# Performance work log

Measured on AMD Instinct MI355X. Metric: run time of the kernel, lower is better.

Reference implementation:

```python
import jax, jax.numpy as jnp
import numpy as np

N, E = 20000, 160000
F, H, OUT = 256, 8, 128
L = 6            # total layers -> 5 GAT layers
LM1 = L - 1
NGN = L // 3 + 1 # 3 GraphNorms
D = F // H       # 32 per head
GN_FREQ = 3
EPS = 1e-5


def setup_inputs() -> dict:
    key = jax.random.key(0)
    ks = jax.random.split(key, 12)
    x = jax.random.normal(ks[0], (N, 1), dtype=jnp.float32)
    edge_index = jax.random.randint(ks[1], (2, E), 0, N, dtype=jnp.int32)
    W0 = jax.random.normal(ks[2], (1, F), dtype=jnp.float32) * 0.1
    b0 = jnp.zeros((F,), jnp.float32)
    gat_lin = jax.random.normal(ks[3], (LM1, F, F), dtype=jnp.float32) * (1.0 / np.sqrt(F))
    att_src = jax.random.normal(ks[4], (LM1, H, D), dtype=jnp.float32) * 0.1
    att_dst = jax.random.normal(ks[5], (LM1, H, D), dtype=jnp.float32) * 0.1
    gat_bias = jnp.zeros((LM1, F), jnp.float32)
    gn_weight = jnp.ones((NGN, F), jnp.float32)
    gn_bias = jnp.zeros((NGN, F), jnp.float32)
    gn_mean_scale = jnp.ones((NGN, F), jnp.float32)
    lin_W = jax.random.normal(ks[6], (F, OUT), dtype=jnp.float32) * (1.0 / np.sqrt(F))
    lin_b = jnp.zeros((OUT,), jnp.float32)
    return {"x": x, "W0": W0, "b0": b0, "gat_lin": gat_lin, "att_src": att_src,
            "att_dst": att_dst, "gat_bias": gat_bias, "gn_weight": gn_weight,
            "gn_bias": gn_bias, "gn_mean_scale": gn_mean_scale,
            "lin_W": lin_W, "lin_b": lin_b, "edge_index": edge_index}


def _gcn_conv(x, W, b, src, dst, n):
    h = x @ W
    deg = jax.ops.segment_sum(jnp.ones(src.shape[0], h.dtype), dst, num_segments=n)
    dinv = jnp.where(deg > 0, jax.lax.rsqrt(deg), 0.0)
    norm = dinv[src] * dinv[dst]                      # [E']
    out = jax.ops.segment_sum(h[src] * norm[:, None], dst, num_segments=n)
    return out + b


def _gat_conv(x, W, a_src, a_dst, src, dst, n):
    # PyG GATConv (concat=True, negative_slope=0.2, self-loops in src/dst)
    h = (x @ W).reshape(n, H, D)
    s = jnp.einsum('nhd,hd->nh', h, a_src)            # [N,H]
    t = jnp.einsum('nhd,hd->nh', h, a_dst)
    e = jax.nn.leaky_relu(s[src] + t[dst], 0.2)       # [E',H]
    m = jax.ops.segment_max(e, dst, num_segments=n)   # per-dst softmax
    e = jnp.exp(e - m[dst])
    denom = jax.ops.segment_sum(e, dst, num_segments=n)
    alpha = e / (denom[dst] + 1e-16)
    out = jax.ops.segment_sum(h[src] * alpha[:, :, None], dst, num_segments=n)
    return out.reshape(n, F)


def _graph_norm(x, w, b, ms):
    # PyG GraphNorm with batch=None (single graph): per-feature stats over nodes
    mean = jnp.mean(x, axis=0)
    out = x - ms * mean
    var = jnp.mean(out * out, axis=0)
    return w * out * jax.lax.rsqrt(var + EPS) + b


def reference(x, W0, b0, gat_lin, att_src, att_dst, gat_bias, gn_weight, gn_bias,
              gn_mean_scale, lin_W, lin_b, edge_index):
    n = x.shape[0]
    loops = jnp.arange(n, dtype=edge_index.dtype)
    src = jnp.concatenate([edge_index[0], loops])
    dst = jnp.concatenate([edge_index[1], loops])
    h = jax.nn.relu(_gcn_conv(x, W0, b0, src, dst, n))
    for i in range(LM1):
        if i % GN_FREQ == 0:
            g = i // GN_FREQ
            h = _graph_norm(h, gn_weight[g], gn_bias[g], gn_mean_scale[g])
        out = _gat_conv(h, gat_lin[i], att_src[i], att_dst[i], src, dst, n)
        if i % GN_FREQ == 0:
            out = out + gat_bias[i]
        h = h + jax.nn.relu(out)
    return h @ lin_W + lin_b
```

## Files before the change

kernel.cpp:

```cpp
#include <hip/hip_runtime.h>
#include <hip/hip_bf16.h>
#include <stdint.h>

typedef float f32x4 __attribute__((ext_vector_type(4)));
typedef short s16x8 __attribute__((ext_vector_type(8)));

__device__ __forceinline__ float bf2f(unsigned short u) {
    union { unsigned int i; float f; } v; v.i = ((unsigned int)u) << 16; return v.f;
}
__device__ __forceinline__ unsigned short f2bf(float f) {
    union { float f; unsigned int i; } v; v.f = f;
    unsigned int x = v.i;
    return (unsigned short)((x + 0x7fffu + ((x >> 16) & 1u)) >> 16);
}
__device__ __forceinline__ void bfp(unsigned int u, float& lo, float& hi) {
    union { unsigned int i; float f; } a, b;
    a.i = u << 16; b.i = u & 0xffff0000u;
    lo = a.f; hi = b.f;
}
__device__ __forceinline__ void gload16(const void* g, void* l) {
    __builtin_amdgcn_global_load_lds(
        (const __attribute__((address_space(1))) void*)g,
        (__attribute__((address_space(3))) void*)l, 16, 0, 0);
}

__global__ void k_count(const int* __restrict__ ei, int E, int* deg) {
    int e = blockIdx.x * blockDim.x + threadIdx.x;
    if (e < E) atomicAdd(&deg[ei[E + e]], 1);
}

__global__ __launch_bounds__(256) void k_bsum(const int* __restrict__ deg,
                                              int* __restrict__ bsum, int n) {
    __shared__ int buf[256];
    int i = blockIdx.x * 256 + threadIdx.x;
    buf[threadIdx.x] = (i < n) ? deg[i] + 1 : 0;
    __syncthreads();
#pragma unroll
    for (int off = 128; off > 0; off >>= 1) {
        if ((int)threadIdx.x < off) buf[threadIdx.x] += buf[threadIdx.x + off];
        __syncthreads();
    }
    if (threadIdx.x == 0) bsum[blockIdx.x] = buf[0];
}

__global__ __launch_bounds__(256) void k_scanb(const int* __restrict__ bsum,
                                               int* __restrict__ boff, int nb) {
    __shared__ int buf[256];
    int t = threadIdx.x;
    int v = (t < nb) ? bsum[t] : 0;
    buf[t] = v;
    __syncthreads();
    for (int off = 1; off < 256; off <<= 1) {
        int add = (t >= off) ? buf[t - off] : 0;
        __syncthreads();
        buf[t] += add;
        __syncthreads();
    }
    if (t < nb) boff[t] = buf[t] - v;
}

__global__ __launch_bounds__(256) void k_emit(const int* __restrict__ deg,
                                              const int* __restrict__ boff,
                                              int* __restrict__ rowptr,
                                              int* __restrict__ wo,
                                              float* __restrict__ dinv, int n) {
    __shared__ int buf[256];
    int i = blockIdx.x * 256 + threadIdx.x;
    int v = (i < n) ? deg[i] + 1 : 0;
    buf[threadIdx.x] = v;
    __syncthreads();
    for (int off = 1; off < 256; off <<= 1) {
        int add = ((int)threadIdx.x >= off) ? buf[threadIdx.x - off] : 0;
        __syncthreads();
        buf[threadIdx.x] += add;
        __syncthreads();
    }
    if (i < n) {
        int excl = boff[blockIdx.x] + buf[threadIdx.x] - v;
        rowptr[i] = excl;
        wo[i] = excl;
        dinv[i] = rsqrtf((float)v);
        if (i == n - 1) rowptr[n] = excl + v;
    }
}

__global__ void k_fill(const int* __restrict__ ei, int E, int n,
                       int* wo, int* srcs) {
    int e = blockIdx.x * blockDim.x + threadIdx.x;
    int EP = E + n;
    if (e >= EP) return;
    int s_, d_;
    if (e < E) { s_ = ei[e]; d_ = ei[E + e]; }
    else       { s_ = d_ = e - E; }
    int pos = atomicAdd(&wo[d_], 1);
    srcs[pos] = s_;
}

__global__ __launch_bounds__(256) void k_h0f(const float* __restrict__ x,
                                             const float* __restrict__ dinv,
                                             const int* __restrict__ rowptr,
                                             const int* __restrict__ srcs,
                                             const float* __restrict__ W0,
                                             const float* __restrict__ b0,
                                             unsigned short* __restrict__ hbf,
                                             int n, int Mpad) {
    int wave = threadIdx.x >> 6, lane = threadIdx.x & 63;
    int node = blockIdx.x * 4 + wave;
    if (node >= Mpad) return;
    size_t base = (size_t)node * 256 + lane * 4;
    if (node >= n) {
        ushort4 z = {0, 0, 0, 0};
        *reinterpret_cast<ushort4*>(hbf + base) = z;
        return;
    }
    int p0 = rowptr[node], p1 = rowptr[node + 1];
    float sum = 0.f;
    for (int p = p0 + lane; p < p1; p += 64) {
        int s = srcs[p];
        sum += x[s] * dinv[s];
    }
#pragma unroll
    for (int m = 1; m < 64; m <<= 1) sum += __shfl_xor(sum, m);
    float sv = sum * dinv[node];
    float4 wv = *reinterpret_cast<const float4*>(W0 + lane * 4);
    float4 bv = *reinterpret_cast<const float4*>(b0 + lane * 4);
    ushort4 o;
    o.x = f2bf(fmaxf(sv * wv.x + bv.x, 0.f));
    o.y = f2bf(fmaxf(sv * wv.y + bv.y, 0.f));
    o.z = f2bf(fmaxf(sv * wv.z + bv.z, 0.f));
    o.w = f2bf(fmaxf(sv * wv.w + bv.w, 0.f));
    *reinterpret_cast<ushort4*>(hbf + base) = o;
}

__global__ void k_wprep(const float* __restrict__ gat_lin,
                        const float* __restrict__ lin_W,
                        const float* __restrict__ att_src,
                        const float* __restrict__ att_dst,
                        unsigned short* __restrict__ Wt,
                        unsigned short* __restrict__ lt) {
    int idx = blockIdx.x * blockDim.x + threadIdx.x;
    const int T1 = 5 * 65536;
    const int T2 = T1 + 128 * 256;
    const int T3 = T2 + 5 * 64 * 256;
    if (idx < T1) {
        int l = idx >> 16, r = idx & 0xFFFF;
        int nrow = r >> 8, k = r & 255;
        Wt[(size_t)l * 81920 + nrow * 256 + k] =
            f2bf(gat_lin[(size_t)l * 65536 + k * 256 + nrow]);
    } else if (idx < T2) {
        int j = idx - T1;
        int nrow = j >> 8, k = j & 255;
        lt[nrow * 256 + k] = f2bf(lin_W[(size_t)k * 128 + nrow]);
    } else if (idx < T3) {
        int j = idx - T2;
        int l = j >> 14, r = j & 16383;
        int row = r >> 8, k = r & 255;
        float v = 0.f;
        if (row < 16) {
            int head = row & 7;
            const float* a = (row < 8) ? (att_src + l * 256 + head * 32)
                                       : (att_dst + l * 256 + head * 32);
            const float* wr = gat_lin + (size_t)l * 65536 + k * 256 + head * 32;
#pragma unroll
            for (int d = 0; d < 32; ++d) v += wr[d] * a[d];
        }
        Wt[(size_t)l * 81920 + (256 + row) * 256 + k] = f2bf(v);
    }
}

__global__ __launch_bounds__(256) void k_gn_reduce(const unsigned short* __restrict__ hbf,
                                                   float* sums, float* sumsq, int n) {
    int f = threadIdx.x;
    float s = 0.f, q = 0.f;
    for (int r = blockIdx.x; r < n; r += gridDim.x) {
        float v = bf2f(hbf[(size_t)r * 256 + f]);
        s += v; q += v * v;
    }
    atomicAdd(&sums[f], s);
    atomicAdd(&sumsq[f], q);
}

__global__ __launch_bounds__(256) void k_gnfold(const float* __restrict__ st,
                                                const float* __restrict__ w,
                                                const float* __restrict__ b,
                                                const float* __restrict__ ms,
                                                unsigned short* __restrict__ Wt,
                                                float* __restrict__ so,
                                                float* __restrict__ rowbias,
                                                float ninv) {
    __shared__ float red[256];
    int col = blockIdx.x, k = threadIdx.x;
    float mean = st[k] * ninv;
    float m2   = st[256 + k] * ninv;
    float msf  = ms[k];
    float var  = m2 + msf * mean * mean * (msf - 2.0f);
    float sc = w[k] * rsqrtf(var + 1e-5f);
    float of = b[k] - msf * mean * sc;
    size_t idx = (size_t)col * 256 + k;
    float wv = bf2f(Wt[idx]);
    red[k] = of * wv;
    __syncthreads();
#pragma unroll
    for (int off = 128; off > 0; off >>= 1) {
        if (k < off) red[k] += red[k + off];
        __syncthreads();
    }
    if (k == 0) rowbias[col] = red[0];
    Wt[idx] = f2bf(sc * wv);
    if (col == 0) { so[k] = sc; so[256 + k] = of; }
}

#define BM 64
__global__ __launch_bounds__(512) void k_gemm_mfma(
    const unsigned short* __restrict__ A,
    const unsigned short* __restrict__ Bt,
    unsigned short* __restrict__ Cb,
    float* __restrict__ Cf,
    float* __restrict__ sbuf,
    float* __restrict__ tbuf,
    const float* __restrict__ bias,
    const float* __restrict__ rowbias,
    int M, int ldc)
{
    __shared__ unsigned short As[64 * 256];
    __shared__ unsigned short Bs[64 * 256];
    const int tid = threadIdx.x;
    const int bm = blockIdx.x * BM;
    const int bn = blockIdx.y * 64;
    {
        const char* ga = (const char*)(A + (size_t)bm * 256);
        const char* gb = (const char*)(Bt + (size_t)bn * 256);
        char* la = (char*)As;
        char* lb = (char*)Bs;
#pragma unroll
        for (int i = 0; i < 4; ++i) {
            int o  = (i * 512 + tid) * 16;
            int so = o ^ (((o >> 9) & 7) << 4);
            gload16(ga + so, la + o);
            gload16(gb + so, lb + o);
        }
    }
    __syncthreads();

    const int lane = tid & 63;
    const int w  = tid >> 6;
    const int wm = (w >> 1) * 16;
    const int wn = (w & 1) * 32;
    const int r  = lane & 15, kb = lane >> 4;
    const int r4 = (lane >> 4) * 4, cc = lane & 15;
    const char* la = (const char*)As;
    const char* lb = (const char*)Bs;

    f32x4 acc[2] = {};
#pragma unroll
    for (int ks = 0; ks < 8; ++ks) {
        int row = wm + r;
        int c16 = (ks * 4 + kb) ^ (row & 7);
        s16x8 af = *(const s16x8*)(la + row * 512 + c16 * 16);
#pragma unroll
        for (int j = 0; j < 2; ++j) {
            int col = wn + j * 16 + r;
            int d16 = (ks * 4 + kb) ^ (col & 7);
            s16x8 bfr = *(const s16x8*)(lb + col * 512 + d16 * 16);
            acc[j] = __builtin_amdgcn_mfma_f32_16x16x32_bf16(af, bfr, acc[j], 0, 0, 0);
        }
    }
#pragma unroll
    for (int j = 0; j < 2; ++j) {
        int col = bn + wn + j * 16 + cc;
        float rb = rowbias ? rowbias[col] : 0.f;
#pragma unroll
        for (int q = 0; q < 4; ++q) {
            int row = bm + wm + r4 + q;
            float v = acc[j][q] + rb;
            if (Cb) {
                if (col < 256) {
                    Cb[(size_t)row * 256 + col] = f2bf(v);
                } else if (col < 264) {
                    sbuf[(size_t)row * 8 + (col - 256)] = v;
                } else if (col < 272) {
                    tbuf[(size_t)row * 8 + (col - 264)] = v;
                }
            } else if (row < M) {
                Cf[(size_t)row * ldc + col] = v + bias[col];
            }
        }
    }
}

__global__ __launch_bounds__(256) void k_fagg(const unsigned short* __restrict__ h1,
                                              const float* __restrict__ sbuf,
                                              const float* __restrict__ tbuf,
                                              const int* __restrict__ rowptr,
                                              const int* __restrict__ srcs,
                                              unsigned short* __restrict__ hbf,
                                              const float* __restrict__ bias,
                                              const float* __restrict__ so, int n) {
    int wave = threadIdx.x >> 6, lane = threadIdx.x & 63;
    int node = blockIdx.x * 4 + wave;
    if (node >= n) return;
    int p0 = rowptr[node], p1 = rowptr[node + 1];
    int hid = lane >> 5;
    int l5 = lane & 31;
    int fl = l5 * 8;
    int head = l5 >> 2;
    float tv = tbuf[node * 8 + head];
    float m = -1e30f, den = 0.f;
    float a0 = 0.f, a1 = 0.f, a2 = 0.f, a3 = 0.f;
    float a4 = 0.f, a5 = 0.f, a6 = 0.f, a7 = 0.f;
    int q = p0 + hid;
    for (; q + 2 < p1; q += 4) {
        int s0 = srcs[q], s1 = srcs[q + 2];
        float e0 = sbuf[s0 * 8 + head] + tv;
        float e1 = sbuf[s1 * 8 + head] + tv;
        uint4 v0 = *reinterpret_cast<const uint4*>(h1 + (size_t)s0 * 256 + fl);
        uint4 v1 = *reinterpret_cast<const uint4*>(h1 + (size_t)s1 * 256 + fl);
        e0 = (e0 > 0.f) ? e0 : 0.2f * e0;
        e1 = (e1 > 0.f) ? e1 : 0.2f * e1;
        float mn = fmaxf(m, fmaxf(e0, e1));
        float sc = __expf(m - mn);
        float w0 = __expf(e0 - mn), w1 = __expf(e1 - mn);
        den = den * sc + (w0 + w1);
        float f0l, f0h, f1l, f1h;
        bfp(v0.x, f0l, f0h); bfp(v1.x, f1l, f1h);
        a0 = fmaf(a0, sc, w0 * f0l + w1 * f1l);
        a1 = fmaf(a1, sc, w0 * f0h + w1 * f1h);
        bfp(v0.y, f0l, f0h); bfp(v1.y, f1l, f1h);
        a2 = fmaf(a2, sc, w0 * f0l + w1 * f1l);
        a3 = fmaf(a3, sc, w0 * f0h + w1 * f1h);
        bfp(v0.z, f0l, f0h); bfp(v1.z, f1l, f1h);
        a4 = fmaf(a4, sc, w0 * f0l + w1 * f1l);
        a5 = fmaf(a5, sc, w0 * f0h + w1 * f1h);
        bfp(v0.w, f0l, f0h); bfp(v1.w, f1l, f1h);
        a6 = fmaf(a6, sc, w0 * f0l + w1 * f1l);
        a7 = fmaf(a7, sc, w0 * f0h + w1 * f1h);
        m = mn;
    }
    for (; q < p1; q += 2) {
        int s0 = srcs[q];
        float e0 = sbuf[s0 * 8 + head] + tv;
        uint4 v0 = *reinterpret_cast<const uint4*>(h1 + (size_t)s0 * 256 + fl);
        e0 = (e0 > 0.f) ? e0 : 0.2f * e0;
        float mn = fmaxf(m, e0);
        float sc = __expf(m - mn);
        float w0 = __expf(e0 - mn);
        den = den * sc + w0;
        float f0l, f0h;
        bfp(v0.x, f0l, f0h);
        a0 = fmaf(a0, sc, w0 * f0l); a1 = fmaf(a1, sc, w0 * f0h);
        bfp(v0.y, f0l, f0h);
        a2 = fmaf(a2, sc, w0 * f0l); a3 = fmaf(a3, sc, w0 * f0h);
        bfp(v0.z, f0l, f0h);
        a4 = fmaf(a4, sc, w0 * f0l); a5 = fmaf(a5, sc, w0 * f0h);
        bfp(v0.w, f0l, f0h);
        a6 = fmaf(a6, sc, w0 * f0l); a7 = fmaf(a7, sc, w0 * f0h);
        m = mn;
    }
    float mo = __shfl_xor(m, 32);
    float mm = fmaxf(m, mo);
    float sc = __expf(m - mm);
    den *= sc; den += __shfl_xor(den, 32);
    a0 *= sc; a0 += __shfl_xor(a0, 32);
    a1 *= sc; a1 += __shfl_xor(a1, 32);
    a2 *= sc; a2 += __shfl_xor(a2, 32);
    a3 *= sc; a3 += __shfl_xor(a3, 32);
    a4 *= sc; a4 += __shfl_xor(a4, 32);
    a5 *= sc; a5 += __shfl_xor(a5, 32);
    a6 *= sc; a6 += __shfl_xor(a6, 32);
    a7 *= sc; a7 += __shfl_xor(a7, 32);
    if (hid) return;
    float inv = 1.0f / (den + 1e-16f);
    a0 *= inv; a1 *= inv; a2 *= inv; a3 *= inv;
    a4 *= inv; a5 *= inv; a6 *= inv; a7 *= inv;
    float b_[8] = {0.f, 0.f, 0.f, 0.f, 0.f, 0.f, 0.f, 0.f};
    if (bias) {
        float4 blo = *reinterpret_cast<const float4*>(bias + fl);
        float4 bhi = *reinterpret_cast<const float4*>(bias + fl + 4);
        b_[0] = blo.x; b_[1] = blo.y; b_[2] = blo.z; b_[3] = blo.w;
        b_[4] = bhi.x; b_[5] = bhi.y; b_[6] = bhi.z; b_[7] = bhi.w;
    }
    size_t base = (size_t)node * 256 + fl;
    uint4 hv = *reinterpret_cast<const uint4*>(hbf + base);
    float h_[8];
    bfp(hv.x, h_[0], h_[1]); bfp(hv.y, h_[2], h_[3]);
    bfp(hv.z, h_[4], h_[5]); bfp(hv.w, h_[6], h_[7]);
    if (so) {
        float4 s0v = *reinterpret_cast<const float4*>(so + fl);
        float4 s1v = *reinterpret_cast<const float4*>(so + fl + 4);
        float4 o0v = *reinterpret_cast<const float4*>(so + 256 + fl);
        float4 o1v = *reinterpret_cast<const float4*>(so + 256 + fl + 4);
        h_[0] = h_[0] * s0v.x + o0v.x; h_[1] = h_[1] * s0v.y + o0v.y;
        h_[2] = h_[2] * s0v.z + o0v.z; h_[3] = h_[3] * s0v.w + o0v.w;
        h_[4] = h_[4] * s1v.x + o1v.x; h_[5] = h_[5] * s1v.y + o1v.y;
        h_[6] = h_[6] * s1v.z + o1v.z; h_[7] = h_[7] * s1v.w + o1v.w;
    }
    float r0 = h_[0] + fmaxf(a0 + b_[0], 0.f);
    float r1 = h_[1] + fmaxf(a1 + b_[1], 0.f);
    float r2 = h_[2] + fmaxf(a2 + b_[2], 0.f);
    float r3 = h_[3] + fmaxf(a3 + b_[3], 0.f);
    float r4 = h_[4] + fmaxf(a4 + b_[4], 0.f);
    float r5 = h_[5] + fmaxf(a5 + b_[5], 0.f);
    float r6 = h_[6] + fmaxf(a6 + b_[6], 0.f);
    float r7 = h_[7] + fmaxf(a7 + b_[7], 0.f);
    uint4 o;
    o.x = (unsigned int)f2bf(r0) | ((unsigned int)f2bf(r1) << 16);
    o.y = (unsigned int)f2bf(r2) | ((unsigned int)f2bf(r3) << 16);
    o.z = (unsigned int)f2bf(r4) | ((unsigned int)f2bf(r5) << 16);
    o.w = (unsigned int)f2bf(r6) | ((unsigned int)f2bf(r7) << 16);
    *reinterpret_cast<uint4*>(hbf + base) = o;
}

extern "C" void kernel_launch(void* const* d_in, const int* in_sizes, int n_in,
                              void* d_out, int out_size, void* d_ws, size_t ws_size,
                              hipStream_t stream) {
    const float* x        = (const float*)d_in[0];
    const float* W0       = (const float*)d_in[1];
    const float* b0       = (const float*)d_in[2];
    const float* gat_lin  = (const float*)d_in[3];
    const float* att_src  = (const float*)d_in[4];
    const float* att_dst  = (const float*)d_in[5];
    const float* gat_bias = (const float*)d_in[6];
    const float* gn_w     = (const float*)d_in[7];
    const float* gn_b     = (const float*)d_in[8];
    const float* gn_ms    = (const float*)d_in[9];
    const float* lin_W    = (const float*)d_in[10];
    const float* lin_b    = (const float*)d_in[11];
    const int*   ei       = (const int*)d_in[12];

    const int n  = in_sizes[0];
    const int E  = in_sizes[12] / 2;
    const int EP = E + n;
    const int Mpad = ((n + BM - 1) / BM) * BM;
    const int nb = (n + 255) / 256;

    char* w = (char*)d_ws;
    unsigned short* hbf = (unsigned short*)w; w += (size_t)Mpad * 256 * 2;
    unsigned short* h1  = (unsigned short*)w; w += (size_t)Mpad * 256 * 2;
    float* sbuf = (float*)w;                  w += (size_t)Mpad * 8 * 4;
    float* tbuf = (float*)w;                  w += (size_t)Mpad * 8 * 4;
    unsigned short* Wt = (unsigned short*)w;  w += (size_t)5 * 320 * 256 * 2;
    unsigned short* lt = (unsigned short*)w;  w += (size_t)128 * 256 * 2;
    float* scaleoff = (float*)w;              w += 1024 * 4;
    float* rowbias  = (float*)w;              w += 640 * 4;
    float* gnstat = (float*)w;                w += 1024 * 4;
    int* deg    = (int*)w;                    w += (size_t)n * 4;
    float* dinv = (float*)w;                  w += (size_t)n * 4;
    int* rowptr = (int*)w;                    w += ((size_t)(n + 1) * 4 + 15) / 16 * 16;
    int* wo     = (int*)w;                    w += (size_t)n * 4;
    int* bsum   = (int*)w;                    w += ((size_t)nb * 4 + 15) / 16 * 16;
    int* boff   = (int*)w;                    w += ((size_t)nb * 4 + 15) / 16 * 16;
    int* srcs   = (int*)w;                    w += (size_t)EP * 4;

    const int B256 = 256;
    auto cdiv = [](int a, int b) { return (a + b - 1) / b; };

    hipMemsetAsync(gnstat, 0, 1024 * 4 + (size_t)n * 4, stream);

    const int WPREP = 5 * 65536 + 128 * 256 + 5 * 64 * 256;
    k_wprep<<<cdiv(WPREP, B256), B256, 0, stream>>>(gat_lin, lin_W, att_src, att_dst, Wt, lt);

    k_count<<<cdiv(E, B256), B256, 0, stream>>>(ei, E, deg);
    k_bsum<<<nb, 256, 0, stream>>>(deg, bsum, n);
    k_scanb<<<1, 256, 0, stream>>>(bsum, boff, nb);
    k_emit<<<nb, 256, 0, stream>>>(deg, boff, rowptr, wo, dinv, n);
    k_fill<<<cdiv(EP, B256), B256, 0, stream>>>(ei, E, n, wo, srcs);

    k_h0f<<<cdiv(Mpad, 4), 256, 0, stream>>>(x, dinv, rowptr, srcs, W0, b0, hbf, n, Mpad);

    const float ninv = 1.0f / (float)n;
    const int gx = Mpad / BM;

    for (int i = 0; i < 5; ++i) {
        const float* rb = nullptr;
        const float* so = nullptr;
        if (i % 3 == 0) {
            int g = i / 3;
            k_gn_reduce<<<256, 256, 0, stream>>>(hbf, gnstat + g * 512,
                                                 gnstat + g * 512 + 256, n);
            k_gnfold<<<320, 256, 0, stream>>>(gnstat + g * 512, gn_w + g * 256,
                                              gn_b + g * 256, gn_ms + g * 256,
                                              Wt + (size_t)i * 81920,
                                              scaleoff + g * 512, rowbias + g * 320, ninv);
            rb = rowbias + g * 320;
            so = scaleoff + g * 512;
        }
        k_gemm_mfma<<<dim3(gx, 5), 512, 0, stream>>>(
            hbf, Wt + (size_t)i * 81920, h1, nullptr, sbuf, tbuf, nullptr, rb,
            n, 256);
        k_fagg<<<cdiv(n, 4), 256, 0, stream>>>(
            h1, sbuf, tbuf, rowptr, srcs, hbf,
            (i % 3 == 0) ? gat_bias + i * 256 : nullptr, so, n);
    }

    k_gemm_mfma<<<dim3(gx, 2), 512, 0, stream>>>(
        hbf, lt, nullptr, (float*)d_out, nullptr, nullptr, lin_b, nullptr,
        n, 128);
}
```

Measured before the change: 286.7 us.

## Two-pass GAT softmax with precomputed max; merge degree count into weight prep

The GAT aggregation kernel now computes the per-head segment max in a first pass over neighbor scores, with 8 heads by 8 edge slots per wave. The main loop then accumulates exp weights without online rescaling and is unrolled to four edges per half-wave. This removes the per-edge max/rescale exp and the cross-half rescale, at the cost of re-reading srcs and sbuf. Separately, the degree-count kernel is folded into the weight-prep kernel as extra blocks, saving one launch.

```diff
diff --git a/kernel.cpp b/kernel.cpp
--- a/kernel.cpp
+++ b/kernel.cpp
@@ -24,121 +24,21 @@
         (__attribute__((address_space(3))) void*)l, 16, 0, 0);
 }
 
-__global__ void k_count(const int* __restrict__ ei, int E, int* deg) {
-    int e = blockIdx.x * blockDim.x + threadIdx.x;
-    if (e < E) atomicAdd(&deg[ei[E + e]], 1);
-}
-
-__global__ __launch_bounds__(256) void k_bsum(const int* __restrict__ deg,
-                                              int* __restrict__ bsum, int n) {
-    __shared__ int buf[256];
-    int i = blockIdx.x * 256 + threadIdx.x;
-    buf[threadIdx.x] = (i < n) ? deg[i] + 1 : 0;
-    __syncthreads();
-#pragma unroll
-    for (int off = 128; off > 0; off >>= 1) {
-        if ((int)threadIdx.x < off) buf[threadIdx.x] += buf[threadIdx.x + off];
-        __syncthreads();
-    }
-    if (threadIdx.x == 0) bsum[blockIdx.x] = buf[0];
-}
-
-__global__ __launch_bounds__(256) void k_scanb(const int* __restrict__ bsum,
-                                               int* __restrict__ boff, int nb) {
-    __shared__ int buf[256];
-    int t = threadIdx.x;
-    int v = (t < nb) ? bsum[t] : 0;
-    buf[t] = v;
-    __syncthreads();
-    for (int off = 1; off < 256; off <<= 1) {
-        int add = (t >= off) ? buf[t - off] : 0;
-        __syncthreads();
-        buf[t] += add;
-        __syncthreads();
-    }
-    if (t < nb) boff[t] = buf[t] - v;
-}
-
-__global__ __launch_bounds__(256) void k_emit(const int* __restrict__ deg,
-                                              const int* __restrict__ boff,
-                                              int* __restrict__ rowptr,
-                                              int* __restrict__ wo,
-                                              float* __restrict__ dinv, int n) {
-    __shared__ int buf[256];
-    int i = blockIdx.x * 256 + threadIdx.x;
-    int v = (i < n) ? deg[i] + 1 : 0;
-    buf[threadIdx.x] = v;
-    __syncthreads();
-    for (int off = 1; off < 256; off <<= 1) {
-        int add = ((int)threadIdx.x >= off) ? buf[threadIdx.x - off] : 0;
-        __syncthreads();
-        buf[threadIdx.x] += add;
-        __syncthreads();
-    }
-    if (i < n) {
-        int excl = boff[blockIdx.x] + buf[threadIdx.x] - v;
-        rowptr[i] = excl;
-        wo[i] = excl;
-        dinv[i] = rsqrtf((float)v);
-        if (i == n - 1) rowptr[n] = excl + v;
-    }
-}
-
-__global__ void k_fill(const int* __restrict__ ei, int E, int n,
-                       int* wo, int* srcs) {
-    int e = blockIdx.x * blockDim.x + threadIdx.x;
-    int EP = E + n;
-    if (e >= EP) return;
-    int s_, d_;
-    if (e < E) { s_ = ei[e]; d_ = ei[E + e]; }
-    else       { s_ = d_ = e - E; }
-    int pos = atomicAdd(&wo[d_], 1);
-    srcs[pos] = s_;
-}
-
-__global__ __launch_bounds__(256) void k_h0f(const float* __restrict__ x,
-                                             const float* __restrict__ dinv,
-                                             const int* __restrict__ rowptr,
-                                             const int* __restrict__ srcs,
-                                             const float* __restrict__ W0,
-                                             const float* __restrict__ b0,
-                                             unsigned short* __restrict__ hbf,
-                                             int n, int Mpad) {
-    int wave = threadIdx.x >> 6, lane = threadIdx.x & 63;
-    int node = blockIdx.x * 4 + wave;
-    if (node >= Mpad) return;
-    size_t base = (size_t)node * 256 + lane * 4;
-    if (node >= n) {
-        ushort4 z = {0, 0, 0, 0};
-        *reinterpret_cast<ushort4*>(hbf + base) = z;
+__global__ void k_prep(const int* __restrict__ ei, int E, int* __restrict__ deg,
+                       int CB,
+                       const float* __restrict__ gat_lin,
+                       const float* __restrict__ lin_W,
+                       const float* __restrict__ att_src,
+                       const float* __restrict__ att_dst,
+                       unsigned short* __restrict__ Wt,
+                       unsigned short* __restrict__ lt) {
+    int bid = blockIdx.x;
+    if (bid < CB) {
+        int e = bid * 256 + threadIdx.x;
+        if (e < E) atomicAdd(&deg[ei[E + e]], 1);
         return;
     }
-    int p0 = rowptr[node], p1 = rowptr[node + 1];
-    float sum = 0.f;
-    for (int p = p0 + lane; p < p1; p += 64) {
-        int s = srcs[p];
-        sum += x[s] * dinv[s];
-    }
-#pragma unroll
-    for (int m = 1; m < 64; m <<= 1) sum += __shfl_xor(sum, m);
-    float sv = sum * dinv[node];
-    float4 wv = *reinterpret_cast<const float4*>(W0 + lane * 4);
-    float4 bv = *reinterpret_cast<const float4*>(b0 + lane * 4);
-    ushort4 o;
-    o.x = f2bf(fmaxf(sv * wv.x + bv.x, 0.f));
-    o.y = f2bf(fmaxf(sv * wv.y + bv.y, 0.f));
-    o.z = f2bf(fmaxf(sv * wv.z + bv.z, 0.f));
-    o.w = f2bf(fmaxf(sv * wv.w + bv.w, 0.f));
-    *reinterpret_cast<ushort4*>(hbf + base) = o;
-}
-
-__global__ void k_wprep(const float* __restrict__ gat_lin,
-                        const float* __restrict__ lin_W,
-                        const float* __restrict__ att_src,
-                        const float* __restrict__ att_dst,
-                        unsigned short* __restrict__ Wt,
-                        unsigned short* __restrict__ lt) {
-    int idx = blockIdx.x * blockDim.x + threadIdx.x;
+    int idx = (bid - CB) * 256 + threadIdx.x;
     const int T1 = 5 * 65536;
     const int T2 = T1 + 128 * 256;
     const int T3 = T2 + 5 * 64 * 256;
@@ -168,6 +68,109 @@
     }
 }
 
+__global__ __launch_bounds__(256) void k_bsum(const int* __restrict__ deg,
+                                              int* __restrict__ bsum, int n) {
+    __shared__ int buf[256];
+    int i = blockIdx.x * 256 + threadIdx.x;
+    buf[threadIdx.x] = (i < n) ? deg[i] + 1 : 0;
+    __syncthreads();
+#pragma unroll
+    for (int off = 128; off > 0; off >>= 1) {
+        if ((int)threadIdx.x < off) buf[threadIdx.x] += buf[threadIdx.x + off];
+        __syncthreads();
+    }
+    if (threadIdx.x == 0) bsum[blockIdx.x] = buf[0];
+}
+
+__global__ __launch_bounds__(256) void k_scanb(const int* __restrict__ bsum,
+                                               int* __restrict__ boff, int nb) {
+    __shared__ int buf[256];
+    int t = threadIdx.x;
+    int v = (t < nb) ? bsum[t] : 0;
+    buf[t] = v;
+    __syncthreads();
+    for (int off = 1; off < 256; off <<= 1) {
+        int add = (t >= off) ? buf[t - off] : 0;
+        __syncthreads();
+        buf[t] += add;
+        __syncthreads();
+    }
+    if (t < nb) boff[t] = buf[t] - v;
+}
+
+__global__ __launch_bounds__(256) void k_emit(const int* __restrict__ deg,
+                                              const int* __restrict__ boff,
+                                              int* __restrict__ rowptr,
+                                              int* __restrict__ wo,
+                                              float* __restrict__ dinv, int n) {
+    __shared__ int buf[256];
+    int i = blockIdx.x * 256 + threadIdx.x;
+    int v = (i < n) ? deg[i] + 1 : 0;
+    buf[threadIdx.x] = v;
+    __syncthreads();
+    for (int off = 1; off < 256; off <<= 1) {
+        int add = ((int)threadIdx.x >= off) ? buf[threadIdx.x - off] : 0;
+        __syncthreads();
+        buf[threadIdx.x] += add;
+        __syncthreads();
+    }
+    if (i < n) {
+        int excl = boff[blockIdx.x] + buf[threadIdx.x] - v;
+        rowptr[i] = excl;
+        wo[i] = excl;
+        dinv[i] = rsqrtf((float)v);
+        if (i == n - 1) rowptr[n] = excl + v;
+    }
+}
+
+__global__ void k_fill(const int* __restrict__ ei, int E, int n,
+                       int* wo, int* srcs) {
+    int e = blockIdx.x * blockDim.x + threadIdx.x;
+    int EP = E + n;
+    if (e >= EP) return;
+    int s_, d_;
+    if (e < E) { s_ = ei[e]; d_ = ei[E + e]; }
+    else       { s_ = d_ = e - E; }
+    int pos = atomicAdd(&wo[d_], 1);
+    srcs[pos] = s_;
+}
+
+__global__ __launch_bounds__(256) void k_h0f(const float* __restrict__ x,
+                                             const float* __restrict__ dinv,
+                                             const int* __restrict__ rowptr,
+                                             const int* __restrict__ srcs,
+                                             const float* __restrict__ W0,
+                                             const float* __restrict__ b0,
+                                             unsigned short* __restrict__ hbf,
+                                             int n, int Mpad) {
+    int wave = threadIdx.x >> 6, lane = threadIdx.x & 63;
+    int node = blockIdx.x * 4 + wave;
+    if (node >= Mpad) return;
+    size_t base = (size_t)node * 256 + lane * 4;
+    if (node >= n) {
+        ushort4 z = {0, 0, 0, 0};
+        *reinterpret_cast<ushort4*>(hbf + base) = z;
+        return;
+    }
+    int p0 = rowptr[node], p1 = rowptr[node + 1];
+    float sum = 0.f;
+    for (int p = p0 + lane; p < p1; p += 64) {
+        int s = srcs[p];
+        sum += x[s] * dinv[s];
+    }
+#pragma unroll
+    for (int m = 1; m < 64; m <<= 1) sum += __shfl_xor(sum, m);
+    float sv = sum * dinv[node];
+    float4 wv = *reinterpret_cast<const float4*>(W0 + lane * 4);
+    float4 bv = *reinterpret_cast<const float4*>(b0 + lane * 4);
+    ushort4 o;
+    o.x = f2bf(fmaxf(sv * wv.x + bv.x, 0.f));
+    o.y = f2bf(fmaxf(sv * wv.y + bv.y, 0.f));
+    o.z = f2bf(fmaxf(sv * wv.z + bv.z, 0.f));
+    o.w = f2bf(fmaxf(sv * wv.w + bv.w, 0.f));
+    *reinterpret_cast<ushort4*>(hbf + base) = o;
+}
+
 __global__ __launch_bounds__(256) void k_gn_reduce(const unsigned short* __restrict__ hbf,
                                                    float* sums, float* sumsq, int n) {
     int f = threadIdx.x;
@@ -300,74 +303,80 @@
     int node = blockIdx.x * 4 + wave;
     if (node >= n) return;
     int p0 = rowptr[node], p1 = rowptr[node + 1];
+
+    int h8 = lane & 7;
+    int slot = lane >> 3;
+    float tv1 = tbuf[node * 8 + h8];
+    float m = -1e30f;
+    for (int p = p0 + slot; p < p1; p += 8) {
+        int s = srcs[p];
+        float e = sbuf[s * 8 + h8] + tv1;
+        e = (e > 0.f) ? e : 0.2f * e;
+        m = fmaxf(m, e);
+    }
+    m = fmaxf(m, __shfl_xor(m, 8));
+    m = fmaxf(m, __shfl_xor(m, 16));
+    m = fmaxf(m, __shfl_xor(m, 32));
+
     int hid = lane >> 5;
     int l5 = lane & 31;
     int fl = l5 * 8;
     int head = l5 >> 2;
+    float mh = __shfl(m, head);
     float tv = tbuf[node * 8 + head];
-    float m = -1e30f, den = 0.f;
+    float den = 0.f;
     float a0 = 0.f, a1 = 0.f, a2 = 0.f, a3 = 0.f;
     float a4 = 0.f, a5 = 0.f, a6 = 0.f, a7 = 0.f;
     int q = p0 + hid;
-    for (; q + 2 < p1; q += 4) {
-        int s0 = srcs[q], s1 = srcs[q + 2];
+    for (; q + 6 < p1; q += 8) {
+        int s0 = srcs[q], s1 = srcs[q + 2], s2 = srcs[q + 4], s3 = srcs[q + 6];
         float e0 = sbuf[s0 * 8 + head] + tv;
         float e1 = sbuf[s1 * 8 + head] + tv;
+        float e2 = sbuf[s2 * 8 + head] + tv;
+        float e3 = sbuf[s3 * 8 + head] + tv;
         uint4 v0 = *reinterpret_cast<const uint4*>(h1 + (size_t)s0 * 256 + fl);
         uint4 v1 = *reinterpret_cast<const uint4*>(h1 + (size_t)s1 * 256 + fl);
+        uint4 v2 = *reinterpret_cast<const uint4*>(h1 + (size_t)s2 * 256 + fl);
+        uint4 v3 = *reinterpret_cast<const uint4*>(h1 + (size_t)s3 * 256 + fl);
         e0 = (e0 > 0.f) ? e0 : 0.2f * e0;
         e1 = (e1 > 0.f) ? e1 : 0.2f * e1;
-        float mn = fmaxf(m, fmaxf(e0, e1));
-        float sc = __expf(m - mn);
-        float w0 = __expf(e0 - mn), w1 = __expf(e1 - mn);
-        den = den * sc + (w0 + w1);
-        float f0l, f0h, f1l, f1h;
-        bfp(v0.x, f0l, f0h); bfp(v1.x, f1l, f1h);
-        a0 = fmaf(a0, sc, w0 * f0l + w1 * f1l);
-        a1 = fmaf(a1, sc, w0 * f0h + w1 * f1h);
-        bfp(v0.y, f0l, f0h); bfp(v1.y, f1l, f1h);
-        a2 = fmaf(a2, sc, w0 * f0l + w1 * f1l);
-        a3 = fmaf(a3, sc, w0 * f0h + w1 * f1h);
-        bfp(v0.z, f0l, f0h); bfp(v1.z, f1l, f1h);
-        a4 = fmaf(a4, sc, w0 * f0l + w1 * f1l);
-        a5 = fmaf(a5, sc, w0 * f0h + w1 * f1h);
-        bfp(v0.w, f0l, f0h); bfp(v1.w, f1l, f1h);
-        a6 = fmaf(a6, sc, w0 * f0l + w1 * f1l);
-        a7 = fmaf(a7, sc, w0 * f0h + w1 * f1h);
-        m = mn;
+        e2 = (e2 > 0.f) ? e2 : 0.2f * e2;
+        e3 = (e3 > 0.f) ? e3 : 0.2f * e3;
+        float w0 = __expf(e0 - mh), w1 = __expf(e1 - mh);
+        float w2 = __expf(e2 - mh), w3 = __expf(e3 - mh);
+        den += (w0 + w1) + (w2 + w3);
+        float fl0, fh0, fl1, fh1, fl2, fh2, fl3, fh3;
+        bfp(v0.x, fl0, fh0); bfp(v1.x, fl1, fh1); bfp(v2.x, fl2, fh2); bfp(v3.x, fl3, fh3);
+        a0 += (w0 * fl0 + w1 * fl1) + (w2 * fl2 + w3 * fl3);
+        a1 += (w0 * fh0 + w1 * fh1) + (w2 * fh2 + w3 * fh3);
+        bfp(v0.y, fl0, fh0); bfp(v1.y, fl1, fh1); bfp(v2.y, fl2, fh2); bfp(v3.y, fl3, fh3);
+        a2 += (w0 * fl0 + w1 * fl1) + (w2 * fl2 + w3 * fl3);
+        a3 += (w0 * fh0 + w1 * fh1) + (w2 * fh2 + w3 * fh3);
+        bfp(v0.z, fl0, fh0); bfp(v1.z, fl1, fh1); bfp(v2.z, fl2, fh2); bfp(v3.z, fl3, fh3);
+        a4 += (w0 * fl0 + w1 * fl1) + (w2 * fl2 + w3 * fl3);
+        a5 += (w0 * fh0 + w1 * fh1) + (w2 * fh2 + w3 * fh3);
+        bfp(v0.w, fl0, fh0); bfp(v1.w, fl1, fh1); bfp(v2.w, fl2, fh2); bfp(v3.w, fl3, fh3);
+        a6 += (w0 * fl0 + w1 * fl1) + (w2 * fl2 + w3 * fl3);
+        a7 += (w0 * fh0 + w1 * fh1) + (w2 * fh2 + w3 * fh3);
     }
     for (; q < p1; q += 2) {
         int s0 = srcs[q];
         float e0 = sbuf[s0 * 8 + head] + tv;
         uint4 v0 = *reinterpret_cast<const uint4*>(h1 + (size_t)s0 * 256 + fl);
         e0 = (e0 > 0.f) ? e0 : 0.2f * e0;
-        float mn = fmaxf(m, e0);
-        float sc = __expf(m - mn);
-        float w0 = __expf(e0 - mn);
-        den = den * sc + w0;
-        float f0l, f0h;
-        bfp(v0.x, f0l, f0h);
-        a0 = fmaf(a0, sc, w0 * f0l); a1 = fmaf(a1, sc, w0 * f0h);
-        bfp(v0.y, f0l, f0h);
-        a2 = fmaf(a2, sc, w0 * f0l); a3 = fmaf(a3, sc, w0 * f0h);
-        bfp(v0.z, f0l, f0h);
-        a4 = fmaf(a4, sc, w0 * f0l); a5 = fmaf(a5, sc, w0 * f0h);
-        bfp(v0.w, f0l, f0h);
-        a6 = fmaf(a6, sc, w0 * f0l); a7 = fmaf(a7, sc, w0 * f0h);
-        m = mn;
-    }
-    float mo = __shfl_xor(m, 32);
-    float mm = fmaxf(m, mo);
-    float sc = __expf(m - mm);
-    den *= sc; den += __shfl_xor(den, 32);
-    a0 *= sc; a0 += __shfl_xor(a0, 32);
-    a1 *= sc; a1 += __shfl_xor(a1, 32);
-    a2 *= sc; a2 += __shfl_xor(a2, 32);
-    a3 *= sc; a3 += __shfl_xor(a3, 32);
-    a4 *= sc; a4 += __shfl_xor(a4, 32);
-    a5 *= sc; a5 += __shfl_xor(a5, 32);
-    a6 *= sc; a6 += __shfl_xor(a6, 32);
-    a7 *= sc; a7 += __shfl_xor(a7, 32);
+        float w0 = __expf(e0 - mh);
+        den += w0;
+        float fl0, fh0;
+        bfp(v0.x, fl0, fh0); a0 += w0 * fl0; a1 += w0 * fh0;
+        bfp(v0.y, fl0, fh0); a2 += w0 * fl0; a3 += w0 * fh0;
+        bfp(v0.z, fl0, fh0); a4 += w0 * fl0; a5 += w0 * fh0;
+        bfp(v0.w, fl0, fh0); a6 += w0 * fl0; a7 += w0 * fh0;
+    }
+    den += __shfl_xor(den, 32);
+    a0 += __shfl_xor(a0, 32); a1 += __shfl_xor(a1, 32);
+    a2 += __shfl_xor(a2, 32); a3 += __shfl_xor(a3, 32);
+    a4 += __shfl_xor(a4, 32); a5 += __shfl_xor(a5, 32);
+    a6 += __shfl_xor(a6, 32); a7 += __shfl_xor(a7, 32);
     if (hid) return;
     float inv = 1.0f / (den + 1e-16f);
     a0 *= inv; a1 *= inv; a2 *= inv; a3 *= inv;
@@ -456,10 +465,11 @@
 
     hipMemsetAsync(gnstat, 0, 1024 * 4 + (size_t)n * 4, stream);
 
+    const int CB = cdiv(E, B256);
     const int WPREP = 5 * 65536 + 128 * 256 + 5 * 64 * 256;
-    k_wprep<<<cdiv(WPREP, B256), B256, 0, stream>>>(gat_lin, lin_W, att_src, att_dst, Wt, lt);
-
-    k_count<<<cdiv(E, B256), B256, 0, stream>>>(ei, E, deg);
+    k_prep<<<CB + cdiv(WPREP, B256), B256, 0, stream>>>(
+        ei, E, deg, CB, gat_lin, lin_W, att_src, att_dst, Wt, lt);
+
     k_bsum<<<nb, 256, 0, stream>>>(deg, bsum, n);
     k_scanb<<<1, 256, 0, stream>>>(bsum, boff, nb);
     k_emit<<<nb, 256, 0, stream>>>(deg, boff, rowptr, wo, dinv, n);
```

Result: slower. 296.8 us (+3.5%).
